# Kernel tuning notes

Measured on AMD Instinct MI355X. Metric: run time of the kernel, lower is better.

The kernel has to match this reference:

```python
import jax, jax.numpy as jnp
import numpy as np

B, N, D, H, DH, F, L, LC = 32, 256, 512, 8, 64, 2048, 8, 2
NEG = -1e9
SCALE = 1.0 / float(np.sqrt(DH))


def _ln(x, g, b, eps=1e-3):
    # keras LayerNormalization default epsilon=1e-3
    m = jnp.mean(x, -1, keepdims=True)
    v = jnp.mean((x - m) ** 2, -1, keepdims=True)
    return (x - m) * jax.lax.rsqrt(v + eps) * g + b


def setup_inputs() -> dict:
    key = jax.random.key(0)
    ks = jax.random.split(key, 20)
    n = lambda k, s: jax.random.normal(k, s, dtype=jnp.float32) * 0.02
    lengths = jax.random.randint(ks[0], (B,), N // 2, N + 1)
    mask = jnp.arange(N)[None, :] < lengths[:, None]  # [B,N] bool
    return {
        'x': jax.random.normal(ks[1], (B, N, D), dtype=jnp.float32),
        'interaction': jax.random.normal(ks[2], (B, N, N, H), dtype=jnp.float32) * 0.1,
        'class_token': n(ks[3], (1, 1, D)),
        'p_ln1_g': jnp.ones((L, D)), 'p_ln1_b': jnp.zeros((L, D)),
        'p_wq': n(ks[4], (L, D, D)), 'p_wk': n(ks[5], (L, D, D)),
        'p_wv': n(ks[6], (L, D, D)), 'p_wo': n(ks[7], (L, D, D)),
        'p_ln2_g': jnp.ones((L, D)), 'p_ln2_b': jnp.zeros((L, D)),
        'p_w1': n(ks[8], (L, D, F)), 'p_b1': jnp.zeros((L, F)),
        'p_w2': n(ks[9], (L, F, D)), 'p_b2': jnp.zeros((L, D)),
        'c_ln1_g': jnp.ones((LC, D)), 'c_ln1_b': jnp.zeros((LC, D)),
        'c_qk': n(ks[10], (LC, D, H, DH)), 'c_qb': jnp.zeros((LC, H, DH)),
        'c_kk': n(ks[11], (LC, D, H, DH)), 'c_kb': jnp.zeros((LC, H, DH)),
        'c_vk': n(ks[12], (LC, D, H, DH)), 'c_vb': jnp.zeros((LC, H, DH)),
        'c_ok': n(ks[13], (LC, H, DH, D)), 'c_ob': jnp.zeros((LC, D)),
        'c_ln2_g': jnp.ones((LC, D)), 'c_ln2_b': jnp.zeros((LC, D)),
        'c_w1': n(ks[14], (LC, D, F)), 'c_b1': jnp.zeros((LC, F)),
        'c_w2': n(ks[15], (LC, F, D)), 'c_b2': jnp.zeros((LC, D)),
        'mask': mask,
    }


def _part_forward(x, interaction, class_token, p_ln1_g, p_ln1_b, p_wq, p_wk, p_wv, p_wo,
                  p_ln2_g, p_ln2_b, p_w1, p_b1, p_w2, p_b2,
                  c_ln1_g, c_ln1_b, c_qk, c_qb, c_kk, c_kb, c_vk, c_vb, c_ok, c_ob,
                  c_ln2_g, c_ln2_b, c_w1, c_b1, c_w2, c_b2, mask):
    # pairwise particle mask [B,1,N,N]; keras Softmax adds (1-mask)*-1e9
    pmask = (mask[:, None, None, :] & mask[:, None, :, None]).astype(x.dtype)
    padd = (1.0 - pmask) * NEG
    inter = jnp.transpose(interaction, (0, 3, 1, 2))  # [B,H,N,N]
    h = x
    for i in range(L):
        # pre-LN interaction self-attention (dropout inactive at inference)
        hn = _ln(h, p_ln1_g[i], p_ln1_b[i])
        q = (hn @ p_wq[i]).reshape(B, N, H, DH)
        k = (hn @ p_wk[i]).reshape(B, N, H, DH)
        v = (hn @ p_wv[i]).reshape(B, N, H, DH)
        s = jnp.einsum('bqhd,bkhd->bhqk', q, k) * SCALE + inter + padd
        a = jax.nn.softmax(s, axis=-1)
        o = jnp.einsum('bhqk,bkhd->bqhd', a, v).reshape(B, N, D) @ p_wo[i]
        h = h + o
        # pre-LN FFN, gelu (exact, tf.nn.gelu default)
        fn = _ln(h, p_ln2_g[i], p_ln2_b[i])
        h = h + (jax.nn.gelu(fn @ p_w1[i] + p_b1[i], approximate=False) @ p_w2[i] + p_b2[i])
    query = jnp.broadcast_to(class_token, (B, 1, D)).astype(x.dtype)
    cmask = jnp.concatenate([jnp.ones((B, 1), bool), mask], axis=1)[:, None, None, :].astype(x.dtype)
    cadd = (1.0 - cmask) * NEG  # [B,1,1,N+1]
    for i in range(LC):
        # class-attention: K/V from LN(concat([token, particles])), Q from RAW token (as in source)
        cat = jnp.concatenate([query, h], axis=1)  # [B,N+1,D]
        cn = _ln(cat, c_ln1_g[i], c_ln1_b[i])
        qh = jnp.einsum('bqd,dhk->bqhk', query, c_qk[i]) + c_qb[i]
        kh = jnp.einsum('bsd,dhk->bshk', cn, c_kk[i]) + c_kb[i]
        vh = jnp.einsum('bsd,dhk->bshk', cn, c_vk[i]) + c_vb[i]
        s = jnp.einsum('bqhk,bshk->bhqs', qh, kh) * SCALE + cadd
        a = jax.nn.softmax(s, axis=-1)
        o = jnp.einsum('bhqs,bshk->bqhk', a, vh)
        o = jnp.einsum('bqhk,hkd->bqd', o, c_ok[i]) + c_ob[i]
        query = query + o
        fn = _ln(query, c_ln2_g[i], c_ln2_b[i])
        query = query + (jax.nn.gelu(fn @ c_w1[i] + c_b1[i], approximate=False) @ c_w2[i] + c_b2[i])
    return query  # [B,1,D]


def reference(x, interaction, class_token, p_ln1_g, p_ln1_b, p_wq, p_wk, p_wv, p_wo,
              p_ln2_g, p_ln2_b, p_w1, p_b1, p_w2, p_b2,
              c_ln1_g, c_ln1_b, c_qk, c_qb, c_kk, c_kb, c_vk, c_vb, c_ok, c_ob,
              c_ln2_g, c_ln2_b, c_w1, c_b1, c_w2, c_b2, mask):
    return _part_forward(x, interaction, class_token, p_ln1_g, p_ln1_b, p_wq, p_wk, p_wv, p_wo,
                         p_ln2_g, p_ln2_b, p_w1, p_b1, p_w2, p_b2,
                         c_ln1_g, c_ln1_b, c_qk, c_qb, c_kk, c_kb, c_vk, c_vb, c_ok, c_ob,
                         c_ln2_g, c_ln2_b, c_w1, c_b1, c_w2, c_b2, mask)
```

## Files before the change

kernel.cpp:

```cpp
#include <hip/hip_runtime.h>
#include <hip/hip_fp16.h>

#define B_ 32
#define N_ 256
#define D_ 512
#define H_ 8
#define DH_ 64
#define F_ 2048
#define L_ 8
#define LC_ 2
#define NEG_ (-1e9f)
#define SCALE_ 0.125f
#define LDSK 72
#define KCH_ 128

typedef unsigned short u16;
typedef unsigned int u32;
typedef long long s64;
typedef __attribute__((ext_vector_type(8))) short bf16x8;
typedef __attribute__((ext_vector_type(8))) unsigned short u16x8;
typedef __attribute__((ext_vector_type(4))) float f32x4;

__device__ __forceinline__ float b2f(u16 u) {
    union { u32 i; float f; } v; v.i = ((u32)u) << 16; return v.f;
}
__device__ __forceinline__ u16 f2b(float f) {
    union { float f; u32 i; } v; v.f = f;
    u32 x = v.i;
    u32 r = (x + 0x7FFFu + ((x >> 16) & 1u)) >> 16;
    return (u16)r;
}
__device__ __forceinline__ float h2f(u16 u) {
    __half_raw hr; hr.x = u;
    return __half2float(__half(hr));
}
__device__ __forceinline__ void gld16(u16* lds, const u16* g) {
    __builtin_amdgcn_global_load_lds(
        (const __attribute__((address_space(1))) u16*)g,
        (__attribute__((address_space(3))) u16*)lds, 16, 0, 0);
}
__device__ __forceinline__ float ldf(const void* p, size_t i, int fl) {
    if (fl == 1) return ((const float*)p)[i];
    if (fl == 0) return b2f(((const u16*)p)[i]);
    return h2f(((const u16*)p)[i]);
}
__device__ __forceinline__ void ld4(const void* p, size_t i, int fl, float o[4]) {
    if (fl == 1) {
        const float4 v = *(const float4*)((const float*)p + i);
        o[0] = v.x; o[1] = v.y; o[2] = v.z; o[3] = v.w;
    } else if (fl == 0) {
        const ushort4 v = *(const ushort4*)((const u16*)p + i);
        o[0] = b2f(v.x); o[1] = b2f(v.y); o[2] = b2f(v.z); o[3] = b2f(v.w);
    } else {
        const ushort4 v = *(const ushort4*)((const u16*)p + i);
        o[0] = h2f(v.x); o[1] = h2f(v.y); o[2] = h2f(v.z); o[3] = h2f(v.w);
    }
}

__global__ void sniff_kernel(const u32* __restrict__ g1, int* __restrict__ flag) {
    if (threadIdx.x == 0 && blockIdx.x == 0) {
        u32 w = g1[0];
        int f = 0;
        if (w == 0x3F800000u) f = 1;
        else if (w == 0x3C003C00u) f = 2;
        flag[0] = f;
    }
}

__global__ void mask_decode_kernel(const unsigned char* __restrict__ raw,
                                   float* __restrict__ mf) {
    int i = blockIdx.x * 256 + threadIdx.x;
    if (i >= B_ * N_) return;
    unsigned char c0 = raw[0], c1 = raw[1], c4 = raw[4];
    bool v;
    if (c1 == 0x3F || c1 == 0x3C) {
        v = ((const u16*)raw)[i] != 0;
    } else if (c0 == 1 && c1 == 1) {
        v = raw[i] != 0;
    } else if (c0 == 1 && c1 == 0) {
        if (c4 == 1) v = ((const int*)raw)[i] != 0;
        else v = ((const long long*)raw)[i] != 0;
    } else {
        v = ((const float*)raw)[i] != 0.0f;
    }
    mf[i] = v ? 1.0f : 0.0f;
}

__global__ void cvt_in_kernel(const void* __restrict__ in, float* __restrict__ out,
                              int n, const int* __restrict__ fl) {
    int i = blockIdx.x * 256 + threadIdx.x;
    if (i < n) out[i] = ldf(in, (size_t)i, fl[0]);
}
__global__ void bcast_token_kernel(const void* __restrict__ ct, float* __restrict__ qry,
                                   const int* __restrict__ fl) {
    int i = blockIdx.x * 256 + threadIdx.x;
    qry[i] = ldf(ct, (size_t)(i & (D_ - 1)), fl[0]);
}
__global__ void out_copy_kernel(const float* __restrict__ in, float* __restrict__ out, int n) {
    int i = blockIdx.x * 256 + threadIdx.x;
    if (i < n) out[i] = in[i];
}
__global__ void concat_bias_kernel(const void* __restrict__ b1, s64 o1,
                                   const void* __restrict__ b2, s64 o2,
                                   float* __restrict__ dst, const int* __restrict__ flp) {
    int i = blockIdx.x * 256 + threadIdx.x;
    if (i < 512) dst[i] = ldf(b1, (size_t)(o1 + i), flp[0]);
    else if (i < 1024) dst[i] = ldf(b2, (size_t)(o2 + i - 512), flp[0]);
}

__global__ __launch_bounds__(256) void inter_t_kernel(const void* __restrict__ inter,
                                                      const float* __restrict__ mf,
                                                      u16* __restrict__ out,
                                                      const int* __restrict__ flp) {
    __shared__ float tile[256][9];
    __shared__ float mks[256];
    int fl = flp[0];
    int bq = blockIdx.x;
    int b = bq >> 8, q = bq & 255;
    int t = threadIdx.x;
    size_t base = (size_t)bq * 2048;
#pragma unroll
    for (int p = 0; p < 8; ++p) {
        int e = p * 256 + t;
        tile[e >> 3][e & 7] = ldf(inter, base + e, fl);
    }
    mks[t] = mf[b * 256 + t];
    __syncthreads();
    float mq = mf[b * 256 + q];
    int h = t >> 5;
    int k0 = (t & 31) * 8;
    u16x8 v8;
#pragma unroll
    for (int ii = 0; ii < 8; ++ii) {
        int k = k0 + ii;
        float v = tile[k][h];
        if (mq * mks[k] < 0.5f) v += NEG_;
        v8[ii] = (short)f2b(v);
    }
    *(u16x8*)(out + (((size_t)(b * 8 + h) * 256 + q) * 256 + k0)) = v8;
}

__global__ __launch_bounds__(256) void transpose_w_kernel(const void* __restrict__ W, s64 weoff,
                                                          int Nst, int Kd,
                                                          u16* __restrict__ wt,
                                                          const int* __restrict__ flp) {
    __shared__ float tile[32][33];
    int fl = flp[0];
    int n0 = blockIdx.x * 32, k0 = blockIdx.y * 32;
    int tr = threadIdx.x >> 5, tc = threadIdx.x & 31;
#pragma unroll
    for (int p = 0; p < 4; ++p) {
        int kk = p * 8 + tr;
        tile[kk][tc] = ldf(W, (size_t)(weoff + (s64)(k0 + kk) * Nst + n0 + tc), fl);
    }
    __syncthreads();
#pragma unroll
    for (int p = 0; p < 4; ++p) {
        int nn = p * 8 + tr;
        wt[(s64)(n0 + nn) * Kd + k0 + tc] = f2b(tile[tc][nn]);
    }
}

__global__ __launch_bounds__(256) void twt6_kernel(const void* __restrict__ wq,
                                                   const void* __restrict__ wk,
                                                   const void* __restrict__ wv,
                                                   const void* __restrict__ wo,
                                                   const void* __restrict__ w1,
                                                   const void* __restrict__ w2,
                                                   s64 off44, s64 offw1, s64 offw2,
                                                   u16* __restrict__ wtqkv,
                                                   u16* __restrict__ wto,
                                                   u16* __restrict__ wt1,
                                                   u16* __restrict__ wt2,
                                                   const int* __restrict__ flp) {
    __shared__ float tile[32][33];
    int fl = flp[0];
    int bid = blockIdx.x;
    const void* W; s64 weoff; int Nst, Kd; u16* dst; int lb;
    if (bid < 256)       { W = wq; weoff = off44; Nst = 512;  Kd = 512;  dst = wtqkv;          lb = bid; }
    else if (bid < 512)  { W = wk; weoff = off44; Nst = 512;  Kd = 512;  dst = wtqkv + 262144; lb = bid - 256; }
    else if (bid < 768)  { W = wv; weoff = off44; Nst = 512;  Kd = 512;  dst = wtqkv + 524288; lb = bid - 512; }
    else if (bid < 1024) { W = wo; weoff = off44; Nst = 512;  Kd = 512;  dst = wto;            lb = bid - 768; }
    else if (bid < 2048) { W = w1; weoff = offw1; Nst = 2048; Kd = 512;  dst = wt1;            lb = bid - 1024; }
    else                 { W = w2; weoff = offw2; Nst = 512;  Kd = 2048; dst = wt2;            lb = bid - 2048; }
    int nx = Nst >> 5;
    int n0 = (lb % nx) << 5, k0 = (lb / nx) << 5;
    int tr = threadIdx.x >> 5, tc = threadIdx.x & 31;
#pragma unroll
    for (int p = 0; p < 4; ++p) {
        int kk = p * 8 + tr;
        tile[kk][tc] = ldf(W, (size_t)(weoff + (s64)(k0 + kk) * Nst + n0 + tc), fl);
    }
    __syncthreads();
#pragma unroll
    for (int p = 0; p < 4; ++p) {
        int nn = p * 8 + tr;
        dst[(s64)(n0 + nn) * Kd + k0 + tc] = f2b(tile[tc][nn]);
    }
}

__global__ __launch_bounds__(256) void ln_kernel(const float* __restrict__ in,
                                                 const void* __restrict__ g,
                                                 const void* __restrict__ bta,
                                                 s64 peoff,
                                                 u16* __restrict__ out,
                                                 const int* __restrict__ flp) {
    __shared__ float ws4[4];
    __shared__ float wsq[4];
    int fl = flp[0];
    size_t row = blockIdx.x;
    int t = threadIdx.x;
    float x0 = in[row * D_ + t];
    float x1 = in[row * D_ + 256 + t];
    float s = x0 + x1;
#pragma unroll
    for (int off = 32; off > 0; off >>= 1) s += __shfl_xor(s, off);
    if ((t & 63) == 0) ws4[t >> 6] = s;
    __syncthreads();
    float mean = (ws4[0] + ws4[1] + ws4[2] + ws4[3]) * (1.0f / D_);
    float d0 = x0 - mean, d1 = x1 - mean;
    float sq = d0 * d0 + d1 * d1;
#pragma unroll
    for (int off = 32; off > 0; off >>= 1) sq += __shfl_xor(sq, off);
    if ((t & 63) == 0) wsq[t >> 6] = sq;
    __syncthreads();
    float var = (wsq[0] + wsq[1] + wsq[2] + wsq[3]) * (1.0f / D_);
    float inv = 1.0f / sqrtf(var + 1e-3f);
    out[row * D_ + t]       = f2b(d0 * inv * ldf(g, peoff + t, fl)       + ldf(bta, peoff + t, fl));
    out[row * D_ + 256 + t] = f2b(d1 * inv * ldf(g, peoff + 256 + t, fl) + ldf(bta, peoff + 256 + t, fl));
}

__global__ __launch_bounds__(256) void ln_cat_kernel(const float* __restrict__ qry,
                                                     const float* __restrict__ h,
                                                     const void* __restrict__ g,
                                                     const void* __restrict__ bta,
                                                     s64 peoff,
                                                     u16* __restrict__ out,
                                                     const int* __restrict__ flp) {
    __shared__ float ws4[4];
    __shared__ float wsq[4];
    int fl = flp[0];
    size_t row = blockIdx.x;
    int b = (int)(row / 257);
    int r = (int)(row % 257);
    const float* src = (r == 0) ? (qry + (size_t)b * D_)
                                : (h + ((size_t)b * N_ + (r - 1)) * D_);
    int t = threadIdx.x;
    float x0 = src[t];
    float x1 = src[256 + t];
    float s = x0 + x1;
#pragma unroll
    for (int off = 32; off > 0; off >>= 1) s += __shfl_xor(s, off);
    if ((t & 63) == 0) ws4[t >> 6] = s;
    __syncthreads();
    float mean = (ws4[0] + ws4[1] + ws4[2] + ws4[3]) * (1.0f / D_);
    float d0 = x0 - mean, d1 = x1 - mean;
    float sq = d0 * d0 + d1 * d1;
#pragma unroll
    for (int off = 32; off > 0; off >>= 1) sq += __shfl_xor(sq, off);
    if ((t & 63) == 0) wsq[t >> 6] = sq;
    __syncthreads();
    float var = (wsq[0] + wsq[1] + wsq[2] + wsq[3]) * (1.0f / D_);
    float inv = 1.0f / sqrtf(var + 1e-3f);
    out[row * D_ + t]       = f2b(d0 * inv * ldf(g, peoff + t, fl)       + ldf(bta, peoff + t, fl));
    out[row * D_ + 256 + t] = f2b(d1 * inv * ldf(g, peoff + 256 + t, fl) + ldf(bta, peoff + 256 + t, fl));
}

__global__ __launch_bounds__(512) void mfma_gemm_t(const u16* __restrict__ A,
                                                   const u16* __restrict__ Wt,
                                                   int wst, int wkoff,
                                                   const void* __restrict__ bias, s64 beoff,
                                                   int bflag,
                                                   const float* __restrict__ res,
                                                   void* __restrict__ C, int cbf,
                                                   int M, int N, int K, int act,
                                                   const int* __restrict__ flp) {
    __shared__ u16 Alds[2 * 128 * 64];
    __shared__ u16 Blds[2 * 128 * 64];
    int tid = threadIdx.x;
    int gx = gridDim.x;
    int nwg = gx * gridDim.y;
    int orig = blockIdx.y * gx + blockIdx.x;
    int xcd = orig & 7;
    int qq = nwg >> 3, rr = nwg & 7;
    int wg = (xcd < rr ? xcd * (qq + 1) : rr * (qq + 1) + (xcd - rr) * qq) + (orig >> 3);
    int bx = wg % gx, by = wg / gx;
    int bm = by << 7, bn = bx << 7;
    int wid = tid >> 6, lane = tid & 63;
    int wm = (wid >> 2) << 6, wn = (wid & 3) << 5;
    int l15 = lane & 15, q = lane >> 4;
    f32x4 acc[4][2];
#pragma unroll
    for (int a = 0; a < 4; ++a)
#pragma unroll
        for (int b = 0; b < 2; ++b) acc[a][b] = (f32x4){0.f, 0.f, 0.f, 0.f};
    int srow = tid >> 3;
    int sseg = tid & 7;
    int xseg = sseg ^ (srow & 7);
    const u16* arow[2];
#pragma unroll
    for (int p = 0; p < 2; ++p) {
        int gr = bm + p * 64 + srow;
        if (gr >= M) gr = M - 1;
        arow[p] = A + (size_t)gr * K + (xseg << 3);
    }
    const u16* brow[2];
#pragma unroll
    for (int p = 0; p < 2; ++p)
        brow[p] = Wt + (size_t)(bn + p * 64 + srow) * wst + wkoff + (xseg << 3);
    int dstoff = srow * 64 + (sseg << 3);
    auto stage = [&](int buf, int k0) {
        u16* Ab = Alds + buf * 8192;
        u16* Bb = Blds + buf * 8192;
#pragma unroll
        for (int p = 0; p < 2; ++p) gld16(&Ab[dstoff + p * 4096], arow[p] + k0);
#pragma unroll
        for (int p = 0; p < 2; ++p) gld16(&Bb[dstoff + p * 4096], brow[p] + k0);
    };
    int nt = K >> 6;
    stage(0, 0);
    if (nt > 1) stage(1, 64);
    for (int t = 0; t < nt; ++t) {
        if (t + 1 < nt) asm volatile("s_waitcnt vmcnt(4)" ::: "memory");
        else            asm volatile("s_waitcnt vmcnt(0)" ::: "memory");
        __builtin_amdgcn_s_barrier();
        asm volatile("" ::: "memory");
        const u16* Ac = Alds + (t & 1) * 8192;
        const u16* Bc = Blds + (t & 1) * 8192;
#pragma unroll
        for (int ks = 0; ks < 2; ++ks) {
            int seg = ((ks * 4 + q) ^ (l15 & 7)) << 3;
            bf16x8 af[4], bfr[2];
#pragma unroll
            for (int mt = 0; mt < 4; ++mt)
                af[mt] = *(const bf16x8*)(&Ac[(wm + mt * 16 + l15) * 64 + seg]);
#pragma unroll
            for (int nt2 = 0; nt2 < 2; ++nt2)
                bfr[nt2] = *(const bf16x8*)(&Bc[(wn + nt2 * 16 + l15) * 64 + seg]);
#pragma unroll
            for (int mt = 0; mt < 4; ++mt)
#pragma unroll
                for (int nt2 = 0; nt2 < 2; ++nt2)
                    acc[mt][nt2] = __builtin_amdgcn_mfma_f32_16x16x32_bf16(
                        af[mt], bfr[nt2], acc[mt][nt2], 0, 0, 0);
        }
        asm volatile("" ::: "memory");
        __builtin_amdgcn_s_barrier();
        if (t + 2 < nt) stage(t & 1, (t + 2) << 6);
    }
    int fl = (bflag >= 0) ? bflag : flp[0];
#pragma unroll
    for (int nt2 = 0; nt2 < 2; ++nt2) {
        int col = bn + wn + nt2 * 16 + l15;
        float bv = bias ? ldf(bias, (size_t)(beoff + col), fl) : 0.f;
#pragma unroll
        for (int mt = 0; mt < 4; ++mt) {
#pragma unroll
            for (int i = 0; i < 4; ++i) {
                int row = bm + wm + mt * 16 + q * 4 + i;
                if (row >= M) continue;
                float c = acc[mt][nt2][i] + bv;
                if (act) c = 0.5f * c * (1.0f + erff(c * 0.70710678118654752f));
                if (res) c += res[(size_t)row * N + col];
                if (cbf) ((u16*)C)[(size_t)row * N + col] = f2b(c);
                else     ((float*)C)[(size_t)row * N + col] = c;
            }
        }
    }
}

__global__ __launch_bounds__(256) void skinny_gemm_kernel(const void* __restrict__ A, int abf,
                                                          const void* __restrict__ W, s64 weoff,
                                                          int wst,
                                                          float* __restrict__ Cp,
                                                          int N, int K,
                                                          const int* __restrict__ flp) {
    __shared__ float As[32 * KCH_];
    int wfl = flp[0];
    int tid = threadIdx.x;
    int bn = blockIdx.x << 6;
    int ks = blockIdx.y;
    int k0 = ks * KCH_;
#pragma unroll
    for (int p = 0; p < (32 * KCH_) / 1024; ++p) {
        int idx = p * 1024 + tid * 4;
        int m = idx >> 7, c = idx & (KCH_ - 1);
        size_t gi = (size_t)m * K + k0 + c;
        if (abf) {
            const ushort4 v = *(const ushort4*)((const u16*)A + gi);
            As[idx]     = b2f(v.x);
            As[idx + 1] = b2f(v.y);
            As[idx + 2] = b2f(v.z);
            As[idx + 3] = b2f(v.w);
        } else {
            *(float4*)&As[idx] = *(const float4*)((const float*)A + gi);
        }
    }
    __syncthreads();
    int tx = tid & 63, ty = tid >> 6;
    int n = bn + tx;
    float acc[8] = {0.f, 0.f, 0.f, 0.f, 0.f, 0.f, 0.f, 0.f};
#pragma unroll 4
    for (int kk = 0; kk < KCH_; kk += 4) {
        float w0 = ldf(W, (size_t)(weoff + (s64)(k0 + kk) * wst + n), wfl);
        float w1 = ldf(W, (size_t)(weoff + (s64)(k0 + kk + 1) * wst + n), wfl);
        float w2 = ldf(W, (size_t)(weoff + (s64)(k0 + kk + 2) * wst + n), wfl);
        float w3 = ldf(W, (size_t)(weoff + (s64)(k0 + kk + 3) * wst + n), wfl);
#pragma unroll
        for (int r = 0; r < 8; ++r) {
            const float4 a = *(const float4*)&As[(ty * 8 + r) * KCH_ + kk];
            acc[r] += a.x * w0 + a.y * w1 + a.z * w2 + a.w * w3;
        }
    }
#pragma unroll
    for (int r = 0; r < 8; ++r)
        Cp[((size_t)ks * 32 + ty * 8 + r) * N + n] = acc[r];
}

__global__ __launch_bounds__(256) void skinny_epi_kernel(const float* __restrict__ Cp,
                                                         int KS, int N,
                                                         const void* __restrict__ bias, s64 beoff,
                                                         const float* __restrict__ res,
                                                         float* __restrict__ C, int act,
                                                         const int* __restrict__ flp) {
    int i = blockIdx.x * 256 + threadIdx.x;
    if (i >= 32 * N) return;
    int n = i % N;
    float s = 0.f;
    for (int ks = 0; ks < KS; ++ks) s += Cp[(size_t)ks * 32 * N + i];
    if (bias) s += ldf(bias, (size_t)(beoff + n), flp[0]);
    if (act) s = 0.5f * s * (1.0f + erff(s * 0.70710678118654752f));
    if (res) s += res[i];
    C[i] = s;
}

__global__ __launch_bounds__(256) void attn_mfma_kernel(const u16* __restrict__ QKV,
                                                        const u16* __restrict__ IT,
                                                        u16* __restrict__ O) {
    __shared__ u16 KV[256 * 72];
    __shared__ u16 Amat[64 * 264];
    int bh = blockIdx.y;
    int b = bh >> 3, hh = bh & 7;
    int q0 = blockIdx.x << 6;
    int tid = threadIdx.x;
    int w = tid >> 6, l = tid & 63, q2 = l >> 4, l15 = l & 15;
    {
        int r = tid >> 3, seg = (tid & 7) << 3;
#pragma unroll
        for (int p = 0; p < 8; ++p) {
            int k = p * 32 + r;
            *(u16x8*)(&KV[k * LDSK + seg]) =
                *(const u16x8*)(QKV + (size_t)(b * N_ + k) * 1536 + 512 + hh * DH_ + seg);
        }
    }
    int qrow = q0 + (w << 4) + l15;
    const u16* qptr = QKV + (size_t)(b * N_ + qrow) * 1536 + hh * DH_ + (q2 << 3);
    bf16x8 aq0 = *(const bf16x8*)(qptr);
    bf16x8 aq1 = *(const bf16x8*)(qptr + 32);
    __syncthreads();
    f32x4 acc[16];
#pragma unroll
    for (int t = 0; t < 16; ++t) {
        const u16* kp = &KV[(t * 16 + l15) * LDSK + (q2 << 3)];
        bf16x8 b0 = *(const bf16x8*)(kp);
        bf16x8 b1 = *(const bf16x8*)(kp + 32);
        f32x4 z = (f32x4){0.f, 0.f, 0.f, 0.f};
        z = __builtin_amdgcn_mfma_f32_16x16x32_bf16(aq0, b0, z, 0, 0, 0);
        acc[t] = __builtin_amdgcn_mfma_f32_16x16x32_bf16(aq1, b1, z, 0, 0, 0);
    }
    __syncthreads();
    {
        const u16* vptr = QKV + (size_t)(b * N_ + (w << 6)) * 1536 + 1024 + hh * DH_ + l;
#pragma unroll
        for (int s = 0; s < 8; ++s) {
            u16x8 vv;
#pragma unroll
            for (int e = 0; e < 8; ++e) vv[e] = vptr[(size_t)(s * 8 + e) * 1536];
            *(u16x8*)(&KV[l * 264 + (w << 6) + s * 8]) = vv;
        }
    }
    const u16* itp = IT + ((size_t)bh * N_ + q0 + (w << 4) + (q2 << 2)) * N_ + l15;
    float mx[4] = {-3e38f, -3e38f, -3e38f, -3e38f};
#pragma unroll
    for (int t = 0; t < 16; ++t) {
#pragma unroll
        for (int i = 0; i < 4; ++i) {
            float s = acc[t][i] * SCALE_ + b2f(itp[(size_t)i * N_ + t * 16]);
            acc[t][i] = s;
            mx[i] = fmaxf(mx[i], s);
        }
    }
#pragma unroll
    for (int i = 0; i < 4; ++i) {
        mx[i] = fmaxf(mx[i], __shfl_xor(mx[i], 1));
        mx[i] = fmaxf(mx[i], __shfl_xor(mx[i], 2));
        mx[i] = fmaxf(mx[i], __shfl_xor(mx[i], 4));
        mx[i] = fmaxf(mx[i], __shfl_xor(mx[i], 8));
    }
    float sum[4] = {0.f, 0.f, 0.f, 0.f};
#pragma unroll
    for (int t = 0; t < 16; ++t)
#pragma unroll
        for (int i = 0; i < 4; ++i) {
            float e = expf(acc[t][i] - mx[i]);
            acc[t][i] = e;
            sum[i] += e;
        }
#pragma unroll
    for (int i = 0; i < 4; ++i) {
        sum[i] += __shfl_xor(sum[i], 1);
        sum[i] += __shfl_xor(sum[i], 2);
        sum[i] += __shfl_xor(sum[i], 4);
        sum[i] += __shfl_xor(sum[i], 8);
        sum[i] = 1.0f / sum[i];
    }
#pragma unroll
    for (int t = 0; t < 16; ++t)
#pragma unroll
        for (int i = 0; i < 4; ++i)
            Amat[((w << 4) + (q2 << 2) + i) * 264 + t * 16 + l15] = f2b(acc[t][i] * sum[i]);
    __syncthreads();
    f32x4 pacc[4];
#pragma unroll
    for (int dt = 0; dt < 4; ++dt) pacc[dt] = (f32x4){0.f, 0.f, 0.f, 0.f};
#pragma unroll
    for (int kc = 0; kc < 8; ++kc) {
        bf16x8 af = *(const bf16x8*)(&Amat[((w << 4) + l15) * 264 + kc * 32 + (q2 << 3)]);
#pragma unroll
        for (int dt = 0; dt < 4; ++dt) {
            bf16x8 bf = *(const bf16x8*)(&KV[(dt * 16 + l15) * 264 + kc * 32 + (q2 << 3)]);
            pacc[dt] = __builtin_amdgcn_mfma_f32_16x16x32_bf16(af, bf, pacc[dt], 0, 0, 0);
        }
    }
    u16* ob = O + (size_t)(b * N_ + q0 + (w << 4) + (q2 << 2)) * D_ + hh * DH_ + l15;
#pragma unroll
    for (int dt = 0; dt < 4; ++dt)
#pragma unroll
        for (int i = 0; i < 4; ++i)
            ob[(size_t)i * D_ + dt * 16] = f2b(pacc[dt][i]);
}

__global__ __launch_bounds__(64) void cls_attn_kernel(const float* __restrict__ qh,
                                                      const u16* __restrict__ kvh,
                                                      const float* __restrict__ mf,
                                                      float* __restrict__ O) {
    __shared__ float qs[64];
    __shared__ float am[257];
    int b = blockIdx.x >> 3, hh = blockIdx.x & 7;
    int l = threadIdx.x;
    qs[l] = qh[(size_t)b * D_ + hh * DH_ + l];
    __syncthreads();
    float sv[4];
    float s4 = -1e30f;
    float mx = -1e30f;
#pragma unroll
    for (int jj = 0; jj < 4; ++jj) {
        int j = l + (jj << 6);
        const u16* krow = kvh + (size_t)(b * 257 + j) * 1024 + hh * DH_;
        float s = 0.f;
#pragma unroll 8
        for (int d = 0; d < 64; ++d) s += qs[d] * b2f(krow[d]);
        float cm = (j == 0) ? 1.0f : mf[b * N_ + j - 1];
        s = s * SCALE_ + ((cm > 0.5f) ? 0.0f : NEG_);
        sv[jj] = s;
        mx = fmaxf(mx, s);
    }
    if (l == 0) {
        const u16* krow = kvh + (size_t)(b * 257 + 256) * 1024 + hh * DH_;
        float s = 0.f;
#pragma unroll 8
        for (int d = 0; d < 64; ++d) s += qs[d] * b2f(krow[d]);
        float cm = mf[b * N_ + 255];
        s4 = s * SCALE_ + ((cm > 0.5f) ? 0.0f : NEG_);
        mx = fmaxf(mx, s4);
    }
#pragma unroll
    for (int off = 32; off > 0; off >>= 1) mx = fmaxf(mx, __shfl_xor(mx, off));
    float sum = 0.f;
#pragma unroll
    for (int jj = 0; jj < 4; ++jj) { sv[jj] = expf(sv[jj] - mx); sum += sv[jj]; }
    float e4 = expf(s4 - mx);
    sum += e4;
#pragma unroll
    for (int off = 32; off > 0; off >>= 1) sum += __shfl_xor(sum, off);
    float invs = 1.0f / sum;
#pragma unroll
    for (int jj = 0; jj < 4; ++jj) am[l + (jj << 6)] = sv[jj] * invs;
    if (l == 0) am[256] = e4 * invs;
    __syncthreads();
    float acc = 0.f;
    const u16* vcol = kvh + 512 + hh * DH_ + l;
#pragma unroll 4
    for (int j = 0; j < 257; ++j) acc += am[j] * b2f(vcol[(size_t)(b * 257 + j) * 1024]);
    O[(size_t)b * D_ + hh * DH_ + l] = acc;
}

extern "C" void kernel_launch(void* const* d_in, const int* in_sizes, int n_in,
                              void* d_out, int out_size, void* d_ws, size_t ws_size,
                              hipStream_t stream) {
    const void* x           = d_in[0];
    const void* interaction = d_in[1];
    const void* class_token = d_in[2];
    const void* p_ln1_g = d_in[3];
    const void* p_ln1_b = d_in[4];
    const void* p_wq    = d_in[5];
    const void* p_wk    = d_in[6];
    const void* p_wv    = d_in[7];
    const void* p_wo    = d_in[8];
    const void* p_ln2_g = d_in[9];
    const void* p_ln2_b = d_in[10];
    const void* p_w1    = d_in[11];
    const void* p_b1    = d_in[12];
    const void* p_w2    = d_in[13];
    const void* p_b2    = d_in[14];
    const void* c_ln1_g = d_in[15];
    const void* c_ln1_b = d_in[16];
    const void* c_qk    = d_in[17];
    const void* c_qb    = d_in[18];
    const void* c_kk    = d_in[19];
    const void* c_kb    = d_in[20];
    const void* c_vk    = d_in[21];
    const void* c_vb    = d_in[22];
    const void* c_ok    = d_in[23];
    const void* c_ob    = d_in[24];
    const void* c_ln2_g = d_in[25];
    const void* c_ln2_b = d_in[26];
    const void* c_w1    = d_in[27];
    const void* c_b1    = d_in[28];
    const void* c_w2    = d_in[29];
    const void* c_b2    = d_in[30];
    const unsigned char* maskraw = (const unsigned char*)d_in[31];

    const size_t NT  = (size_t)B_ * N_;
    const size_t NTD = NT * D_;

    char* base = (char*)d_ws;
    int*   flag   = (int*)base;
    float* maskf  = (float*)(base + 64);
    float* h      = (float*)(base + 64 + 32768);
    u16*   hn     = (u16*)(h + NTD);
    u16*   qkv    = hn + (size_t)B_ * 257 * D_;
    float* qry    = (float*)(qkv + (size_t)8192 * 1536);
    float* qh     = qry + 16384;
    float* ocls   = qh + 16384;
    u16*   fnq    = (u16*)(ocls + 16384);
    float* midc   = (float*)(fnq + 16384);
    float* biaskv = midc + 65536;
    u16*   wt     = (u16*)(biaskv + 1024);
    u16*   wtqkv = wt;
    u16*   wto   = wt + 786432;
    u16*   wt1   = wt + 1048576;
    u16*   wt2   = wt + 2097152;
    u16*   inter_t = wt + 3145728;
    u16*   midp  = qkv;
    float* cpart = (float*)(qkv + (size_t)8224 * 1024);

    auto mgemm = [&](const u16* A, const u16* Wt, int wst, int wkoff,
                     const void* bias, s64 beoff, int bflag, const float* res, void* C, int cbf,
                     int M, int N, int K, int act) {
        dim3 grid(N / 128, (M + 127) / 128);
        mfma_gemm_t<<<grid, 512, 0, stream>>>(A, Wt, wst, wkoff, bias, beoff, bflag,
                                              res, C, cbf, M, N, K, act, flag);
    };
    auto skgemm = [&](const void* A, int abf, const void* W, s64 weoff, int wst,
                      const void* bias, s64 beoff, const float* res, float* C,
                      int N, int K, int act) {
        int KS = K / KCH_;
        skinny_gemm_kernel<<<dim3(N / 64, KS), 256, 0, stream>>>(A, abf, W, weoff, wst,
                                                                 cpart, N, K, flag);
        skinny_epi_kernel<<<(32 * N + 255) / 256, 256, 0, stream>>>(cpart, KS, N, bias, beoff,
                                                                    res, C, act, flag);
    };
    auto twt = [&](const void* W, s64 weoff, int Nst, int Kd, u16* dst) {
        dim3 grid(Nst / 32, Kd / 32);
        transpose_w_kernel<<<grid, 256, 0, stream>>>(W, weoff, Nst, Kd, dst, flag);
    };

    sniff_kernel<<<1, 64, 0, stream>>>((const u32*)p_ln1_g, flag);
    mask_decode_kernel<<<32, 256, 0, stream>>>(maskraw, maskf);
    inter_t_kernel<<<8192, 256, 0, stream>>>(interaction, maskf, inter_t, flag);
    cvt_in_kernel<<<(int)(NTD / 256), 256, 0, stream>>>(x, h, (int)NTD, flag);
    bcast_token_kernel<<<64, 256, 0, stream>>>(class_token, qry, flag);

    for (int i = 0; i < L_; ++i) {
        s64 wo = (s64)i * D_ * D_;
        twt6_kernel<<<3072, 256, 0, stream>>>(p_wq, p_wk, p_wv, p_wo, p_w1, p_w2,
                                              wo, (s64)i * D_ * F_, (s64)i * F_ * D_,
                                              wtqkv, wto, wt1, wt2, flag);
        ln_kernel<<<(int)NT, 256, 0, stream>>>(h, p_ln1_g, p_ln1_b, (s64)i * D_, hn, flag);
        mgemm(hn, wtqkv, D_, 0, nullptr, 0, -1, nullptr, qkv, 1, (int)NT, 1536, D_, 0);
        attn_mfma_kernel<<<dim3(4, B_ * H_), 256, 0, stream>>>(qkv, inter_t, hn);
        mgemm(hn, wto, D_, 0, nullptr, 0, -1, h, h, 0, (int)NT, D_, D_, 0);
        ln_kernel<<<(int)NT, 256, 0, stream>>>(h, p_ln2_g, p_ln2_b, (s64)i * D_, hn, flag);
        for (int c = 0; c < 2; ++c) {
            mgemm(hn, wt1 + (s64)c * 1024 * 512, D_, 0,
                  p_b1, (s64)i * F_ + c * 1024, -1, nullptr, midp, 1,
                  (int)NT, 1024, D_, 1);
            mgemm(midp, wt2, F_, c * 1024,
                  (c == 0) ? p_b2 : nullptr, (s64)i * D_, -1, h, h, 0,
                  (int)NT, D_, 1024, 0);
        }
    }

    for (int i = 0; i < LC_; ++i) {
        s64 wo = (s64)i * D_ * D_;
        twt(c_kk, wo, D_, D_, wtqkv);
        twt(c_vk, wo, D_, D_, wtqkv + 262144);
        concat_bias_kernel<<<4, 256, 0, stream>>>(c_kb, (s64)i * D_, c_vb, (s64)i * D_, biaskv, flag);
        ln_cat_kernel<<<B_ * 257, 256, 0, stream>>>(qry, h, c_ln1_g, c_ln1_b, (s64)i * D_, hn, flag);
        skgemm(qry, 0, c_qk, wo, D_, c_qb, (s64)i * D_, nullptr, qh, D_, D_, 0);
        mgemm(hn, wtqkv, D_, 0, biaskv, 0, 1, nullptr, qkv, 1, B_ * 257, 1024, D_, 0);
        cls_attn_kernel<<<B_ * H_, 64, 0, stream>>>(qh, qkv, maskf, ocls);
        skgemm(ocls, 0, c_ok, wo, D_, c_ob, (s64)i * D_, qry, qry, D_, D_, 0);
        ln_kernel<<<B_, 256, 0, stream>>>(qry, c_ln2_g, c_ln2_b, (s64)i * D_, fnq, flag);
        skgemm(fnq, 1, c_w1, (s64)i * D_ * F_, F_, c_b1, (s64)i * F_, nullptr, midc, F_, D_, 1);
        skgemm(midc, 0, c_w2, (s64)i * F_ * D_, D_, c_b2, (s64)i * D_, qry, qry, D_, F_, 0);
    }

    out_copy_kernel<<<(out_size + 255) / 256, 256, 0, stream>>>(qry, (float*)d_out, out_size);
}
```

Before: 2.476 ms.

## Prefetch V and interaction bias into registers before QK MFMA in attention kernel

The attention kernel now issues the global loads for V and for the interaction bias tile into registers before the QK^T MFMA loop, so their latency overlaps the matrix work instead of stalling after it. Full __syncthreads are replaced with lgkmcnt waits plus raw s_barrier, which leaves outstanding vector-memory loads in flight across barriers. The block index is remapped so that consecutive blocks come from different heads and batches, which may change cache locality. The prefetch raises register pressure (64 V values and 64 bias values per thread), which could lower occupancy.

Result: faster. 2.364 ms (-4.5%).

```diff
diff --git a/kernel.cpp b/kernel.cpp
--- a/kernel.cpp
+++ b/kernel.cpp
@@ -439,11 +439,17 @@
                                                         u16* __restrict__ O) {
     __shared__ u16 KV[256 * 72];
     __shared__ u16 Amat[64 * 264];
-    int bh = blockIdx.y;
+    int li = blockIdx.y * 4 + blockIdx.x;
+    int slot = li >> 3;
+    int bh = (li & 7) * 32 + (slot >> 2);
+    int q0 = (slot & 3) << 6;
     int b = bh >> 3, hh = bh & 7;
-    int q0 = blockIdx.x << 6;
     int tid = threadIdx.x;
     int w = tid >> 6, l = tid & 63, q2 = l >> 4, l15 = l & 15;
+    int qrow = q0 + (w << 4) + l15;
+    const u16* qptr = QKV + (size_t)(b * N_ + qrow) * 1536 + hh * DH_ + (q2 << 3);
+    bf16x8 aq0 = *(const bf16x8*)(qptr);
+    bf16x8 aq1 = *(const bf16x8*)(qptr + 32);
     {
         int r = tid >> 3, seg = (tid & 7) << 3;
 #pragma unroll
@@ -453,11 +459,27 @@
                 *(const u16x8*)(QKV + (size_t)(b * N_ + k) * 1536 + 512 + hh * DH_ + seg);
         }
     }
-    int qrow = q0 + (w << 4) + l15;
-    const u16* qptr = QKV + (size_t)(b * N_ + qrow) * 1536 + hh * DH_ + (q2 << 3);
-    bf16x8 aq0 = *(const bf16x8*)(qptr);
-    bf16x8 aq1 = *(const bf16x8*)(qptr + 32);
-    __syncthreads();
+    u16x8 vreg[8];
+    {
+        const u16* vptr = QKV + (size_t)(b * N_ + (w << 6)) * 1536 + 1024 + hh * DH_ + l;
+#pragma unroll
+        for (int s = 0; s < 8; ++s)
+#pragma unroll
+            for (int e = 0; e < 8; ++e)
+                vreg[s][e] = vptr[(size_t)(s * 8 + e) * 1536];
+    }
+    const u16* itp = IT + ((size_t)bh * N_ + q0 + (w << 4) + (q2 << 2)) * N_ + l15;
+    u16 itv0[16], itv1[16], itv2[16], itv3[16];
+#pragma unroll
+    for (int t = 0; t < 16; ++t) {
+        itv0[t] = itp[t * 16];
+        itv1[t] = itp[(size_t)N_ + t * 16];
+        itv2[t] = itp[(size_t)2 * N_ + t * 16];
+        itv3[t] = itp[(size_t)3 * N_ + t * 16];
+    }
+    asm volatile("s_waitcnt lgkmcnt(0)" ::: "memory");
+    __builtin_amdgcn_s_barrier();
+    __builtin_amdgcn_sched_barrier(0);
     f32x4 acc[16];
 #pragma unroll
     for (int t = 0; t < 16; ++t) {
@@ -468,27 +490,24 @@
         z = __builtin_amdgcn_mfma_f32_16x16x32_bf16(aq0, b0, z, 0, 0, 0);
         acc[t] = __builtin_amdgcn_mfma_f32_16x16x32_bf16(aq1, b1, z, 0, 0, 0);
     }
-    __syncthreads();
-    {
-        const u16* vptr = QKV + (size_t)(b * N_ + (w << 6)) * 1536 + 1024 + hh * DH_ + l;
-#pragma unroll
-        for (int s = 0; s < 8; ++s) {
-            u16x8 vv;
-#pragma unroll
-            for (int e = 0; e < 8; ++e) vv[e] = vptr[(size_t)(s * 8 + e) * 1536];
-            *(u16x8*)(&KV[l * 264 + (w << 6) + s * 8]) = vv;
-        }
-    }
-    const u16* itp = IT + ((size_t)bh * N_ + q0 + (w << 4) + (q2 << 2)) * N_ + l15;
+    asm volatile("s_waitcnt lgkmcnt(0)" ::: "memory");
+    __builtin_amdgcn_s_barrier();
+    __builtin_amdgcn_sched_barrier(0);
+#pragma unroll
+    for (int s = 0; s < 8; ++s)
+        *(u16x8*)(&KV[l * 264 + (w << 6) + s * 8]) = vreg[s];
     float mx[4] = {-3e38f, -3e38f, -3e38f, -3e38f};
 #pragma unroll
     for (int t = 0; t < 16; ++t) {
-#pragma unroll
-        for (int i = 0; i < 4; ++i) {
-            float s = acc[t][i] * SCALE_ + b2f(itp[(size_t)i * N_ + t * 16]);
-            acc[t][i] = s;
-            mx[i] = fmaxf(mx[i], s);
-        }
+        float s0 = acc[t][0] * SCALE_ + b2f(itv0[t]);
+        float s1 = acc[t][1] * SCALE_ + b2f(itv1[t]);
+        float s2 = acc[t][2] * SCALE_ + b2f(itv2[t]);
+        float s3 = acc[t][3] * SCALE_ + b2f(itv3[t]);
+        acc[t][0] = s0; acc[t][1] = s1; acc[t][2] = s2; acc[t][3] = s3;
+        mx[0] = fmaxf(mx[0], s0);
+        mx[1] = fmaxf(mx[1], s1);
+        mx[2] = fmaxf(mx[2], s2);
+        mx[3] = fmaxf(mx[3], s3);
     }
 #pragma unroll
     for (int i = 0; i < 4; ++i) {
@@ -519,7 +538,9 @@
 #pragma unroll
         for (int i = 0; i < 4; ++i)
             Amat[((w << 4) + (q2 << 2) + i) * 264 + t * 16 + l15] = f2b(acc[t][i] * sum[i]);
-    __syncthreads();
+    asm volatile("s_waitcnt lgkmcnt(0)" ::: "memory");
+    __builtin_amdgcn_s_barrier();
+    __builtin_amdgcn_sched_barrier(0);
     f32x4 pacc[4];
 #pragma unroll
     for (int dt = 0; dt < 4; ++dt) pacc[dt] = (f32x4){0.f, 0.f, 0.f, 0.f};
```
